# Performance work log

Hardware: AMD Instinct MI355X
Metric: run time of the kernel (lower is better)

Reference implementation:

```python
import jax, jax.numpy as jnp
import numpy as np

B, C, H, W = 4, 64, 128, 128
D_INNER, D_STATE, DT_RANK, K = 192, 16, 6, 4  # d_model = 3*C//2 = 96, expand = 2
EPS = 1e-5


def _haar():
    # pywt db1: dec_lo=[s,s], dec_hi=[-s,s]; code reverses dec_* and uses rec_* in
    # original order -> for Haar both dec and rec filter banks are identical.
    s = np.float32(1.0 / np.sqrt(2.0))
    lo = np.array([s, s], np.float32)
    hi = np.array([s, -s], np.float32)
    # stack order: [lo(i)lo(j), hi(i)lo(j), lo(i)hi(j), hi(i)hi(j)]
    return np.stack([np.outer(lo, lo), np.outer(hi, lo),
                     np.outer(lo, hi), np.outer(hi, hi)], 0)  # (4,2,2)

DEC = jnp.asarray(_haar())
REC = jnp.asarray(_haar())
DN = ('NCHW', 'OIHW', 'NCHW')


def _ln(x, s, b):
    m = x.mean(-1, keepdims=True)
    v = x.var(-1, keepdims=True)
    return (x - m) * jax.lax.rsqrt(v + EPS) * s + b


def _wt(x):
    b, c, h, w = x.shape
    wf = jnp.tile(DEC[:, None], (c, 1, 1, 1))  # (4c,1,2,2), groups=c, pad=0 for db1
    y = jax.lax.conv_general_dilated(x, wf, (2, 2), 'VALID',
                                     feature_group_count=c, dimension_numbers=DN)
    return y.reshape(b, c, 4, h // 2, w // 2)


def _iwt(x):
    # conv_transpose2d(stride=2, pad=0, groups=c) == lhs-dilated conv with flipped kernel, pad k-1
    b, c = x.shape[0], x.shape[1]
    h2, w2 = x.shape[3], x.shape[4]
    xr = x.reshape(b, c * 4, h2, w2)
    wf = jnp.tile(REC[:, ::-1, ::-1][None], (c, 1, 1, 1))  # (c,4,2,2)
    return jax.lax.conv_general_dilated(xr, wf, (1, 1), ((1, 1), (1, 1)),
                                        lhs_dilation=(2, 2), feature_group_count=c,
                                        dimension_numbers=DN)


def _ss2d(x, in_proj_w, conv_dw_w, conv_dw_b, x_proj_w, dt_proj_w, dt_proj_b,
          A_log, Ds, out_norm_s, out_norm_b, out_proj_w):
    b, d, h, w = x.shape  # d == D_INNER
    L = h * w
    xz = jnp.einsum('bchw,ec->behw', x, in_proj_w)  # (b,2d,h,w)
    x1, z = xz[:, :d], xz[:, d:]
    x1 = jax.lax.conv_general_dilated(x1, conv_dw_w, (1, 1), ((1, 1), (1, 1)),
                                      feature_group_count=d, dimension_numbers=DN)
    x1 = jax.nn.silu(x1 + conv_dw_b[None, :, None, None])
    # 4-direction flattening: hw, wh, and their reverses
    xf = x1.reshape(b, d, L)
    xt = x1.transpose(0, 1, 3, 2).reshape(b, d, L)
    xs = jnp.stack([xf, xt], 1)
    xs = jnp.concatenate([xs, xs[..., ::-1]], 1)  # (b,K,d,L)
    x_dbl = jnp.einsum('bkdl,kcd->bkcl', xs, x_proj_w)
    dts = x_dbl[:, :, :DT_RANK]
    Bs = x_dbl[:, :, DT_RANK:DT_RANK + D_STATE]   # (b,K,n,L)
    Cs = x_dbl[:, :, DT_RANK + D_STATE:]
    delta = jax.nn.softplus(jnp.einsum('bkrl,kdr->bkdl', dts, dt_proj_w)
                            + dt_proj_b[None, :, :, None])
    A = -jnp.exp(A_log)  # (K,d,n)

    def step(hc, inp):
        d_t, u_t, b_t, c_t = inp  # (b,K,d),(b,K,d),(b,K,n),(b,K,n)
        dA = jnp.exp(d_t[..., None] * A[None])
        hc = hc * dA + (d_t * u_t)[..., None] * b_t[:, :, None, :]
        y = jnp.einsum('bkdn,bkn->bkd', hc, c_t)
        return hc, y

    h0 = jnp.zeros((b, K, d, D_STATE), x.dtype)
    inputs = (delta.transpose(3, 0, 1, 2), xs.transpose(3, 0, 1, 2),
              Bs.transpose(3, 0, 1, 2), Cs.transpose(3, 0, 1, 2))
    _, ys = jax.lax.scan(step, h0, inputs)            # (L,b,K,d)
    out_y = ys.transpose(1, 2, 3, 0) + xs * Ds[None, :, :, None]  # (b,K,d,L)
    inv_y = out_y[:, 2:][..., ::-1]
    wh = out_y[:, 1].reshape(b, d, w, h).transpose(0, 1, 3, 2).reshape(b, d, L)
    invwh = inv_y[:, 1].reshape(b, d, w, h).transpose(0, 1, 3, 2).reshape(b, d, L)
    y = out_y[:, 0] + inv_y[:, 0] + wh + invwh        # (b,d,L)
    y = _ln(y.reshape(b, d, h, w).transpose(0, 2, 3, 1), out_norm_s, out_norm_b)
    y = y * jax.nn.silu(z.transpose(0, 2, 3, 1))
    y = jnp.einsum('bhwd,ed->bhwe', y, out_proj_w)
    return y.transpose(0, 3, 1, 2)


def reference(x, wt_low_scale, wt_high_scale, low_conv_w, in_proj_w, conv_dw_w,
              conv_dw_b, x_proj_w, dt_proj_w, dt_proj_b, A_log, Ds,
              out_norm_s, out_norm_b, out_proj_w, ln2_s, ln2_b, eca_w):
    b, c = x.shape[0], x.shape[1]
    wt = _wt(x)                                       # (b,c,4,h2,w2)
    h2, w2 = wt.shape[3], wt.shape[4]
    low = wt[:, :, 0] * wt_low_scale
    high = wt[:, :, 1:].reshape(b, c * 3, h2, w2) * wt_high_scale
    low = jax.nn.silu(jnp.einsum('bchw,ec->behw', low, low_conv_w[:, :, 0, 0]))
    high = _ss2d(high, in_proj_w, conv_dw_w, conv_dw_b, x_proj_w, dt_proj_w,
                 dt_proj_b, A_log, Ds, out_norm_s, out_norm_b, out_proj_w)
    high = _ln(high.transpose(0, 2, 3, 1), ln2_s, ln2_b).transpose(0, 3, 1, 2)
    mamba = jnp.tile(low, (1, 3, 1, 1)) * high
    merged = jnp.concatenate([low, mamba], 1).reshape(b, c, 4, h2, w2)
    y = _iwt(merged)                                  # (b,c,h,w)
    # ECA: gap -> conv1d(k=5) over channels -> sigmoid gate
    pooled = y.mean((2, 3))[:, None, :]               # (b,1,c)
    att = jax.lax.conv_general_dilated(pooled, eca_w.reshape(1, 1, 5), (1,),
                                       ((2, 2),), dimension_numbers=('NCH', 'OIH', 'NCH'))
    att = jax.nn.sigmoid(att[:, 0])
    return y * att[:, :, None, None] + x


def setup_inputs():
    key = jax.random.key(0)
    ks = jax.random.split(key, 20)
    f = jax.random.normal
    return {
        'x': f(ks[0], (B, C, H, W), jnp.float32),
        'wt_low_scale': jax.random.uniform(ks[1], (1, C, 1, 1), jnp.float32),
        'wt_high_scale': jax.random.uniform(ks[2], (1, 3 * C, 1, 1), jnp.float32),
        'low_conv_w': f(ks[3], (C, C, 1, 1), jnp.float32) * 0.1,
        'in_proj_w': f(ks[4], (2 * D_INNER, D_INNER), jnp.float32) * 0.05,
        'conv_dw_w': f(ks[5], (D_INNER, 1, 3, 3), jnp.float32) * 0.3,
        'conv_dw_b': f(ks[6], (D_INNER,), jnp.float32) * 0.1,
        'x_proj_w': f(ks[7], (K, DT_RANK + 2 * D_STATE, D_INNER), jnp.float32) * 0.05,
        'dt_proj_w': f(ks[8], (K, D_INNER, DT_RANK), jnp.float32) * 0.1,
        'dt_proj_b': jax.random.uniform(ks[9], (K, D_INNER), jnp.float32) - 4.0,
        'A_log': jax.random.uniform(ks[10], (K, D_INNER, D_STATE), jnp.float32),
        'Ds': f(ks[11], (K, D_INNER), jnp.float32) * 0.1,
        'out_norm_s': jnp.ones((D_INNER,), jnp.float32),
        'out_norm_b': jnp.zeros((D_INNER,), jnp.float32),
        'out_proj_w': f(ks[12], (D_INNER, D_INNER), jnp.float32) * 0.05,
        'ln2_s': jnp.ones((3 * C,), jnp.float32),
        'ln2_b': jnp.zeros((3 * C,), jnp.float32),
        'eca_w': f(ks[13], (5,), jnp.float32) * 0.3,
    }
```

## Files before the change

kernel.cpp:

```cpp
#include <hip/hip_runtime.h>

constexpr int cB = 4, cC = 64, cH = 128, cW = 128;
constexpr int cL = 4096;
constexpr int cD = 192, cN = 16;
constexpr int NCH = 64, CHUNK = 64;

__device__ __forceinline__ float silu_f(float v) { return v / (1.f + __expf(-v)); }

__global__ __launch_bounds__(256) void k_wt(const float* __restrict__ x,
                                            const float* __restrict__ wls,
                                            const float* __restrict__ whs,
                                            float* __restrict__ lraw,
                                            float* __restrict__ high) {
    int idx = blockIdx.x * 256 + threadIdx.x;
    int j = idx & 63, i = (idx >> 6) & 63, c = (idx >> 12) & 63, b = idx >> 18;
    const float* xp = x + (((size_t)(b * cC + c)) * cH + 2 * i) * cW + 2 * j;
    float x00 = xp[0], x01 = xp[1], x10 = xp[cW], x11 = xp[cW + 1];
    float s0 = 0.5f * (x00 + x01 + x10 + x11);
    float s1 = 0.5f * (x00 + x01 - x10 - x11);
    float s2 = 0.5f * (x00 - x01 + x10 - x11);
    float s3 = 0.5f * (x00 - x01 - x10 + x11);
    int l = i * 64 + j;
    lraw[(size_t)(b * cC + c) * cL + l] = s0 * wls[c];
    int ch = c * 3;
    high[(size_t)(b * cD + ch + 0) * cL + l] = s1 * whs[ch + 0];
    high[(size_t)(b * cD + ch + 1) * cL + l] = s2 * whs[ch + 1];
    high[(size_t)(b * cD + ch + 2) * cL + l] = s3 * whs[ch + 2];
}

__global__ __launch_bounds__(256) void k_lowconv(const float* __restrict__ lraw,
                                                 const float* __restrict__ w,
                                                 float* __restrict__ lowT) {
    int bid = blockIdx.x;
    int lt0 = (bid & 63) * 64;
    int b = bid >> 6;
    __shared__ float sW[16][68];
    __shared__ float sI[16][65];
    int tid = threadIdx.x, lt = tid & 63, eg = tid >> 6;
    float acc[16];
#pragma unroll
    for (int m = 0; m < 16; m++) acc[m] = 0.f;
    for (int c0 = 0; c0 < 64; c0 += 16) {
#pragma unroll
        for (int q = 0; q < 4; q++) {
            int tt = tid + q * 256;
            int cc = tt & 15, ee = tt >> 4;
            sW[cc][ee] = w[ee * 64 + c0 + cc];
        }
#pragma unroll
        for (int q = 0; q < 4; q++) {
            int tt = tid + q * 256;
            int ll = tt & 63, cc = tt >> 6;
            sI[cc][ll] = lraw[(size_t)(b * cC + c0 + cc) * cL + lt0 + ll];
        }
        __syncthreads();
#pragma unroll
        for (int cc = 0; cc < 16; cc++) {
            float iv = sI[cc][lt];
#pragma unroll
            for (int m = 0; m < 16; m++) acc[m] = fmaf(sW[cc][eg * 16 + m], iv, acc[m]);
        }
        __syncthreads();
    }
#pragma unroll
    for (int m = 0; m < 16; m++) {
        int e = eg * 16 + m;
        lowT[((size_t)b * cL + lt0 + lt) * 64 + e] = silu_f(acc[m]);
    }
}

__global__ __launch_bounds__(256) void k_inproj(const float* __restrict__ hi,
                                                const float* __restrict__ w,
                                                float* __restrict__ xout,
                                                float* __restrict__ zT) {
    int bid = blockIdx.x;
    int et = bid % 6;
    int blt = bid / 6;
    int lt0 = (blt & 63) * 64;
    int b = blt >> 6;
    int e0 = et * 64;
    __shared__ float sW[16][68];
    __shared__ float sI[16][65];
    int tid = threadIdx.x, lt = tid & 63, eg = tid >> 6;
    float acc[16];
#pragma unroll
    for (int m = 0; m < 16; m++) acc[m] = 0.f;
    for (int c0 = 0; c0 < 192; c0 += 16) {
#pragma unroll
        for (int q = 0; q < 4; q++) {
            int tt = tid + q * 256;
            int cc = tt & 15, ee = tt >> 4;
            sW[cc][ee] = w[(e0 + ee) * 192 + c0 + cc];
        }
#pragma unroll
        for (int q = 0; q < 4; q++) {
            int tt = tid + q * 256;
            int ll = tt & 63, cc = tt >> 6;
            sI[cc][ll] = hi[(size_t)(b * cD + c0 + cc) * cL + lt0 + ll];
        }
        __syncthreads();
#pragma unroll
        for (int cc = 0; cc < 16; cc++) {
            float iv = sI[cc][lt];
#pragma unroll
            for (int m = 0; m < 16; m++) acc[m] = fmaf(sW[cc][eg * 16 + m], iv, acc[m]);
        }
        __syncthreads();
    }
#pragma unroll
    for (int m = 0; m < 16; m++) {
        int e = e0 + eg * 16 + m;
        float v = acc[m];
        if (e < 192) xout[(size_t)(b * cD + e) * cL + lt0 + lt] = v;
        else zT[((size_t)b * cL + lt0 + lt) * 192 + (e - 192)] = v;
    }
}

__global__ __launch_bounds__(256) void k_dwconv(const float* __restrict__ xin,
                                                const float* __restrict__ w,
                                                const float* __restrict__ bias,
                                                float* __restrict__ x1,
                                                float* __restrict__ u1) {
    int bd = blockIdx.x;
    int d = bd % cD;
    const float* xp = xin + (size_t)bd * cL;
    float wv[9];
#pragma unroll
    for (int t = 0; t < 9; t++) wv[t] = w[d * 9 + t];
    float bv = bias[d];
    __shared__ float sm[64][65];
    int tid = threadIdx.x;
#pragma unroll
    for (int q = 0; q < 16; q++) {
        int p = tid + q * 256;
        int i = p >> 6, j = p & 63;
        float acc = bv;
#pragma unroll
        for (int di = 0; di < 3; di++) {
            int ii = i + di - 1;
            if (ii < 0 || ii >= 64) continue;
#pragma unroll
            for (int dj = 0; dj < 3; dj++) {
                int jj = j + dj - 1;
                if (jj < 0 || jj >= 64) continue;
                acc = fmaf(wv[di * 3 + dj], xp[ii * 64 + jj], acc);
            }
        }
        sm[i][j] = silu_f(acc);
    }
    __syncthreads();
#pragma unroll
    for (int q = 0; q < 16; q++) {
        int p = tid + q * 256;
        x1[(size_t)bd * cL + p] = sm[p >> 6][p & 63];
        u1[(size_t)bd * cL + p] = sm[p & 63][p >> 6];
    }
}

__global__ __launch_bounds__(256) void k_xproj(const float* __restrict__ x1,
                                               const float* __restrict__ u1,
                                               const float* __restrict__ xpw,
                                               float* __restrict__ xdbl) {
    int bid = blockIdx.x;
    int lt0 = (bid & 63) * 64;
    int k = (bid >> 6) & 3;
    int b = bid >> 8;
    const float* src = (k & 1) ? u1 : x1;
    bool rev = (k >= 2);
    __shared__ float sW[16][68];
    __shared__ float sI[16][65];
    int tid = threadIdx.x, lt = tid & 63, eg = tid >> 6;
    float acc[16];
#pragma unroll
    for (int m = 0; m < 16; m++) acc[m] = 0.f;
    for (int c0 = 0; c0 < 192; c0 += 16) {
#pragma unroll
        for (int q = 0; q < 4; q++) {
            int tt = tid + q * 256;
            int cc = tt & 15, ee = tt >> 4;
            sW[cc][ee] = (ee < 38) ? xpw[(k * 38 + ee) * 192 + c0 + cc] : 0.f;
        }
#pragma unroll
        for (int q = 0; q < 4; q++) {
            int tt = tid + q * 256;
            int ll = tt & 63, cc = tt >> 6;
            int l = lt0 + ll;
            int lm = rev ? (cL - 1 - l) : l;
            sI[cc][ll] = src[(size_t)(b * cD + c0 + cc) * cL + lm];
        }
        __syncthreads();
#pragma unroll
        for (int cc = 0; cc < 16; cc++) {
            float iv = sI[cc][lt];
#pragma unroll
            for (int m = 0; m < 16; m++) acc[m] = fmaf(sW[cc][eg * 16 + m], iv, acc[m]);
        }
        __syncthreads();
    }
#pragma unroll
    for (int m = 0; m < 16; m++) {
        int e = eg * 16 + m;
        if (e < 38) xdbl[(size_t)((b * 4 + k) * 38 + e) * cL + lt0 + lt] = acc[m];
    }
}

__global__ __launch_bounds__(192) void k_scan1(const float* __restrict__ xdbl,
                                               const float* __restrict__ x1,
                                               const float* __restrict__ u1,
                                               const float* __restrict__ dtw,
                                               const float* __restrict__ dtb,
                                               const float* __restrict__ alog,
                                               float* __restrict__ P,
                                               float* __restrict__ S) {
    int bid = blockIdx.x;
    int ch = bid % NCH;
    int bk = bid / NCH;
    int k = bk & 3, b = bk >> 2;
    int tid = threadIdx.x;
    int d = tid;
    float Av2[16], h[16];
#pragma unroll
    for (int j = 0; j < 16; j++) {
        Av2[j] = -__expf(alog[(k * 192 + d) * 16 + j]) * 1.44269504088896f;
        h[j] = 0.f;
    }
    float dtbv = dtb[k * 192 + d];
    float dtwv[6];
#pragma unroll
    for (int r = 0; r < 6; r++) dtwv[r] = dtw[(k * 192 + d) * 6 + r];
    const float* dtrows = xdbl + (size_t)(bk * 38) * cL;
    const float* Brow = xdbl + (size_t)(bk * 38 + 6) * cL;
    const float* ubase = ((k & 1) ? u1 : x1) + ((size_t)b * cD + d) * cL;
    bool rev = (k >= 2);

    __shared__ float sB[2][16][16];
    __shared__ float sdt[2][16][8];

    int rowA = tid >> 4, colA = tid & 15;
    int p0 = ch * CHUNK;

    for (int idx = tid; idx < 256; idx += 192)
        sB[0][idx & 15][idx >> 4] = Brow[(size_t)(idx >> 4) * cL + p0 + (idx & 15)];
    if (tid < 96) sdt[0][colA][rowA] = dtrows[(size_t)rowA * cL + p0 + colA];

    float Q = 0.f;
    int cur = 0;
    for (int t0 = p0; t0 < p0 + CHUNK; t0 += 16) {
        __syncthreads();
        if (t0 + 16 < p0 + CHUNK) {
            int t1 = t0 + 16;
            for (int idx = tid; idx < 256; idx += 192)
                sB[cur ^ 1][idx & 15][idx >> 4] = Brow[(size_t)(idx >> 4) * cL + t1 + (idx & 15)];
            if (tid < 96) sdt[cur ^ 1][colA][rowA] = dtrows[(size_t)rowA * cL + t1 + colA];
        }
        float uvals[16];
        {
            const float* up = rev ? (ubase + (cL - 16 - t0)) : (ubase + t0);
#pragma unroll
            for (int q = 0; q < 4; q++)
                *reinterpret_cast<float4*>(&uvals[q * 4]) = *reinterpret_cast<const float4*>(up + q * 4);
        }
#pragma unroll
        for (int l = 0; l < 16; l++) {
            float acc = dtbv;
#pragma unroll
            for (int r = 0; r < 6; r++) acc = fmaf(dtwv[r], sdt[cur][l][r], acc);
            float sp = fmaxf(acc, 0.f) + __logf(1.f + __expf(-fabsf(acc)));
            Q += sp;
            float uv = rev ? uvals[15 - l] : uvals[l];
            float duB = sp * uv;
            float Bv[16];
            *reinterpret_cast<float4*>(&Bv[0])  = *reinterpret_cast<const float4*>(&sB[cur][l][0]);
            *reinterpret_cast<float4*>(&Bv[4])  = *reinterpret_cast<const float4*>(&sB[cur][l][4]);
            *reinterpret_cast<float4*>(&Bv[8])  = *reinterpret_cast<const float4*>(&sB[cur][l][8]);
            *reinterpret_cast<float4*>(&Bv[12]) = *reinterpret_cast<const float4*>(&sB[cur][l][12]);
#pragma unroll
            for (int j = 0; j < 16; j++)
                h[j] = fmaf(h[j], exp2f(sp * Av2[j]), duB * Bv[j]);
        }
        cur ^= 1;
    }
    size_t base = (size_t)bid * 16 * 192 + d;
#pragma unroll
    for (int j = 0; j < 16; j++) {
        P[base + (size_t)j * 192] = exp2f(Av2[j] * Q);
        S[base + (size_t)j * 192] = h[j];
    }
}

__global__ __launch_bounds__(256) void k_carry(const float* __restrict__ P,
                                               float* __restrict__ S) {
    int gid = blockIdx.x * 256 + threadIdx.x;
    int d = gid % 192;
    int n = (gid / 192) & 15;
    int bk = gid / 3072;
    float h = 0.f;
    for (int c = 0; c < NCH; c++) {
        size_t idx = ((size_t)(bk * NCH + c) * 16 + n) * 192 + d;
        h = fmaf(P[idx], h, S[idx]);
        S[idx] = h;
    }
}

__global__ __launch_bounds__(192) void k_scan2(const float* __restrict__ xdbl,
                                               const float* __restrict__ x1,
                                               const float* __restrict__ u1,
                                               const float* __restrict__ dtw,
                                               const float* __restrict__ dtb,
                                               const float* __restrict__ alog,
                                               const float* __restrict__ dss,
                                               const float* __restrict__ S,
                                               float* __restrict__ yacc) {
    int bid = blockIdx.x;
    int ch = bid % NCH;
    int bk = bid / NCH;
    int k = bk & 3, b = bk >> 2;
    int tid = threadIdx.x;
    int d = tid;
    float Av2[16], h[16];
#pragma unroll
    for (int j = 0; j < 16; j++) {
        Av2[j] = -__expf(alog[(k * 192 + d) * 16 + j]) * 1.44269504088896f;
        h[j] = (ch == 0) ? 0.f : S[((size_t)(bk * NCH + ch - 1) * 16 + j) * 192 + d];
    }
    float Dv = dss[k * 192 + d];
    float dtbv = dtb[k * 192 + d];
    float dtwv[6];
#pragma unroll
    for (int r = 0; r < 6; r++) dtwv[r] = dtw[(k * 192 + d) * 6 + r];
    const float* dtrows = xdbl + (size_t)(bk * 38) * cL;
    const float* Brow = xdbl + (size_t)(bk * 38 + 6) * cL;
    const float* Crow = xdbl + (size_t)(bk * 38 + 22) * cL;
    const float* ubase = ((k & 1) ? u1 : x1) + ((size_t)b * cD + d) * cL;
    bool rev = (k >= 2);

    __shared__ float sB[2][16][16];
    __shared__ float sC[2][16][16];
    __shared__ float sdt[2][16][8];

    int rowA = tid >> 4, colA = tid & 15;
    int p0 = ch * CHUNK;

    for (int idx = tid; idx < 256; idx += 192) {
        sB[0][idx & 15][idx >> 4] = Brow[(size_t)(idx >> 4) * cL + p0 + (idx & 15)];
        sC[0][idx & 15][idx >> 4] = Crow[(size_t)(idx >> 4) * cL + p0 + (idx & 15)];
    }
    if (tid < 96) sdt[0][colA][rowA] = dtrows[(size_t)rowA * cL + p0 + colA];

    int cur = 0;
    for (int t0 = p0; t0 < p0 + CHUNK; t0 += 16) {
        __syncthreads();
        if (t0 + 16 < p0 + CHUNK) {
            int t1 = t0 + 16;
            for (int idx = tid; idx < 256; idx += 192) {
                sB[cur ^ 1][idx & 15][idx >> 4] = Brow[(size_t)(idx >> 4) * cL + t1 + (idx & 15)];
                sC[cur ^ 1][idx & 15][idx >> 4] = Crow[(size_t)(idx >> 4) * cL + t1 + (idx & 15)];
            }
            if (tid < 96) sdt[cur ^ 1][colA][rowA] = dtrows[(size_t)rowA * cL + t1 + colA];
        }
        float uvals[16];
        {
            const float* up = rev ? (ubase + (cL - 16 - t0)) : (ubase + t0);
#pragma unroll
            for (int q = 0; q < 4; q++)
                *reinterpret_cast<float4*>(&uvals[q * 4]) = *reinterpret_cast<const float4*>(up + q * 4);
        }
#pragma unroll
        for (int l = 0; l < 16; l++) {
            float acc = dtbv;
#pragma unroll
            for (int r = 0; r < 6; r++) acc = fmaf(dtwv[r], sdt[cur][l][r], acc);
            float sp = fmaxf(acc, 0.f) + __logf(1.f + __expf(-fabsf(acc)));
            float uv = rev ? uvals[15 - l] : uvals[l];
            float duB = sp * uv;
            float Bv[16], Cv[16];
            *reinterpret_cast<float4*>(&Bv[0])  = *reinterpret_cast<const float4*>(&sB[cur][l][0]);
            *reinterpret_cast<float4*>(&Bv[4])  = *reinterpret_cast<const float4*>(&sB[cur][l][4]);
            *reinterpret_cast<float4*>(&Bv[8])  = *reinterpret_cast<const float4*>(&sB[cur][l][8]);
            *reinterpret_cast<float4*>(&Bv[12]) = *reinterpret_cast<const float4*>(&sB[cur][l][12]);
            *reinterpret_cast<float4*>(&Cv[0])  = *reinterpret_cast<const float4*>(&sC[cur][l][0]);
            *reinterpret_cast<float4*>(&Cv[4])  = *reinterpret_cast<const float4*>(&sC[cur][l][4]);
            *reinterpret_cast<float4*>(&Cv[8])  = *reinterpret_cast<const float4*>(&sC[cur][l][8]);
            *reinterpret_cast<float4*>(&Cv[12]) = *reinterpret_cast<const float4*>(&sC[cur][l][12]);
            float yA = 0.f, yB = 0.f;
#pragma unroll
            for (int j = 0; j < 8; j++) {
                h[j] = fmaf(h[j], exp2f(sp * Av2[j]), duB * Bv[j]);
                yA = fmaf(h[j], Cv[j], yA);
            }
#pragma unroll
            for (int j = 8; j < 16; j++) {
                h[j] = fmaf(h[j], exp2f(sp * Av2[j]), duB * Bv[j]);
                yB = fmaf(h[j], Cv[j], yB);
            }
            float y = yA + yB + uv * Dv;
            int lg = t0 + l;
            int lm;
            if (k == 0) lm = lg;
            else if (k == 1) lm = (lg & 63) * 64 + (lg >> 6);
            else if (k == 2) lm = cL - 1 - lg;
            else { int qq = cL - 1 - lg; lm = (qq & 63) * 64 + (qq >> 6); }
            atomicAdd(&yacc[((size_t)b * cL + lm) * 192 + d], y);
        }
        cur ^= 1;
    }
}

__global__ __launch_bounds__(256) void k_comb(const float* __restrict__ yacc,
                                              const float* __restrict__ zT,
                                              const float* __restrict__ ons,
                                              const float* __restrict__ onb,
                                              float* __restrict__ yln) {
    int bid = blockIdx.x;
    int b = bid >> 10;
    int pg = bid & 1023;
    int tid = threadIdx.x;
    int wq = tid >> 6, lane = tid & 63;
    int l = pg * 4 + wq;
    float v[3];
    float s = 0.f, s2 = 0.f;
#pragma unroll
    for (int m = 0; m < 3; m++) {
        int d = lane + 64 * m;
        float t = yacc[((size_t)b * cL + l) * 192 + d];
        v[m] = t;
        s += t;
        s2 += t * t;
    }
#pragma unroll
    for (int o = 1; o < 64; o <<= 1) {
        s += __shfl_xor(s, o);
        s2 += __shfl_xor(s2, o);
    }
    float mean = s / 192.f;
    float var = s2 / 192.f - mean * mean;
    float rstd = rsqrtf(var + 1e-5f);
#pragma unroll
    for (int m = 0; m < 3; m++) {
        int d = lane + 64 * m;
        float zv = zT[((size_t)b * cL + l) * 192 + d];
        float yn = (v[m] - mean) * rstd * ons[d] + onb[d];
        yln[((size_t)b * cL + l) * 192 + d] = yn * silu_f(zv);
    }
}

__global__ __launch_bounds__(256) void k_outproj(const float* __restrict__ yln,
                                                 const float* __restrict__ w,
                                                 float* __restrict__ hout) {
    int bid = blockIdx.x;
    int lt0 = (bid & 63) * 64;
    int et = (bid >> 6) % 3;
    int b = bid / 192;
    int e0 = et * 64;
    __shared__ float sW[16][68];
    __shared__ float sI[16][65];
    int tid = threadIdx.x, lt = tid & 63, eg = tid >> 6;
    float acc[16];
#pragma unroll
    for (int m = 0; m < 16; m++) acc[m] = 0.f;
    for (int c0 = 0; c0 < 192; c0 += 16) {
#pragma unroll
        for (int q = 0; q < 4; q++) {
            int tt = tid + q * 256;
            int cc = tt & 15, ee = tt >> 4;
            sW[cc][ee] = w[(e0 + ee) * 192 + c0 + cc];
        }
#pragma unroll
        for (int q = 0; q < 4; q++) {
            int tt = tid + q * 256;
            int cc = tt & 15, lq = tt >> 4;
            sI[cc][lq] = yln[((size_t)b * cL + lt0 + lq) * 192 + c0 + cc];
        }
        __syncthreads();
#pragma unroll
        for (int cc = 0; cc < 16; cc++) {
            float iv = sI[cc][lt];
#pragma unroll
            for (int m = 0; m < 16; m++) acc[m] = fmaf(sW[cc][eg * 16 + m], iv, acc[m]);
        }
        __syncthreads();
    }
#pragma unroll
    for (int m = 0; m < 16; m++) {
        hout[((size_t)b * cL + lt0 + lt) * 192 + e0 + eg * 16 + m] = acc[m];
    }
}

__global__ __launch_bounds__(256) void k_ln2(const float* __restrict__ hout,
                                             const float* __restrict__ lowT,
                                             const float* __restrict__ l2s,
                                             const float* __restrict__ l2b,
                                             float* __restrict__ merged) {
    int bid = blockIdx.x;
    int b = bid >> 10;
    int pg = bid & 1023;
    int tid = threadIdx.x;
    int wq = tid >> 6, lane = tid & 63;
    int l = pg * 4 + wq;
    float v[3];
    float s = 0.f, s2 = 0.f;
#pragma unroll
    for (int m = 0; m < 3; m++) {
        int d = lane + 64 * m;
        float t = hout[((size_t)b * cL + l) * 192 + d];
        v[m] = t;
        s += t;
        s2 += t * t;
    }
#pragma unroll
    for (int o = 1; o < 64; o <<= 1) {
        s += __shfl_xor(s, o);
        s2 += __shfl_xor(s2, o);
    }
    float mean = s / 192.f;
    float var = s2 / 192.f - mean * mean;
    float rstd = rsqrtf(var + 1e-5f);
    float lv = lowT[((size_t)b * cL + l) * 64 + lane];
    float* mp = merged + ((size_t)b * cL + l) * 256;
    mp[lane] = lv;
#pragma unroll
    for (int m = 0; m < 3; m++) {
        int d = lane + 64 * m;
        float hn = (v[m] - mean) * rstd * l2s[d] + l2b[d];
        mp[64 + d] = lv * hn;
    }
}

__global__ __launch_bounds__(256) void k_iwt(const float* __restrict__ merged,
                                             float* __restrict__ ypre) {
    int idx = blockIdx.x * 256 + threadIdx.x;
    int j = idx & 63, i = (idx >> 6) & 63, g = (idx >> 12) & 63, b = idx >> 18;
    const float4 mv = *reinterpret_cast<const float4*>(merged + ((size_t)b * cL + i * 64 + j) * 256 + g * 4);
    float m0 = mv.x, m1 = mv.y, m2 = mv.z, m3 = mv.w;
    float* yp = ypre + ((size_t)(b * 64 + g) * cH + 2 * i) * cW + 2 * j;
    float2 r0 = make_float2(0.5f * (m0 + m1 + m2 + m3), 0.5f * (m0 + m1 - m2 - m3));
    float2 r1 = make_float2(0.5f * (m0 - m1 + m2 - m3), 0.5f * (m0 - m1 - m2 + m3));
    *reinterpret_cast<float2*>(yp) = r0;
    *reinterpret_cast<float2*>(yp + cW) = r1;
}

__global__ __launch_bounds__(256) void k_pool(const float* __restrict__ ypre,
                                              float* __restrict__ pooled) {
    int bg = blockIdx.x;
    const float* p = ypre + (size_t)bg * (cH * cW);
    float s = 0.f;
    for (int t = threadIdx.x; t < cH * cW; t += 256) s += p[t];
#pragma unroll
    for (int o = 1; o < 64; o <<= 1) s += __shfl_xor(s, o);
    __shared__ float red[4];
    if ((threadIdx.x & 63) == 0) red[threadIdx.x >> 6] = s;
    __syncthreads();
    if (threadIdx.x == 0) pooled[bg] = (red[0] + red[1] + red[2] + red[3]) * (1.f / (cH * cW));
}

__global__ __launch_bounds__(256) void k_eca(const float* __restrict__ pooled,
                                             const float* __restrict__ w,
                                             float* __restrict__ att) {
    int t = threadIdx.x;
    int b = t >> 6, c = t & 63;
    float s = 0.f;
#pragma unroll
    for (int u = 0; u < 5; u++) {
        int cc = c + u - 2;
        if (cc >= 0 && cc < 64) s += w[u] * pooled[b * 64 + cc];
    }
    att[t] = 1.f / (1.f + __expf(-s));
}

__global__ __launch_bounds__(256) void k_final(const float* __restrict__ ypre,
                                               const float* __restrict__ x,
                                               const float* __restrict__ att,
                                               float* __restrict__ out) {
    int idx = blockIdx.x * 256 + threadIdx.x;
    size_t base = (size_t)idx * 4;
    int bc = (int)(base >> 14);
    float a = att[bc];
    float4 yv = *reinterpret_cast<const float4*>(ypre + base);
    float4 xv = *reinterpret_cast<const float4*>(x + base);
    float4 o;
    o.x = fmaf(yv.x, a, xv.x);
    o.y = fmaf(yv.y, a, xv.y);
    o.z = fmaf(yv.z, a, xv.z);
    o.w = fmaf(yv.w, a, xv.w);
    *reinterpret_cast<float4*>(out + base) = o;
}

extern "C" void kernel_launch(void* const* d_in, const int* in_sizes, int n_in,
                              void* d_out, int out_size, void* d_ws, size_t ws_size,
                              hipStream_t stream) {
    const float* x    = (const float*)d_in[0];
    const float* wls  = (const float*)d_in[1];
    const float* whs  = (const float*)d_in[2];
    const float* lcw  = (const float*)d_in[3];
    const float* ipw  = (const float*)d_in[4];
    const float* dww  = (const float*)d_in[5];
    const float* dwb  = (const float*)d_in[6];
    const float* xpw  = (const float*)d_in[7];
    const float* dtw  = (const float*)d_in[8];
    const float* dtb  = (const float*)d_in[9];
    const float* alog = (const float*)d_in[10];
    const float* dss  = (const float*)d_in[11];
    const float* ons  = (const float*)d_in[12];
    const float* onb  = (const float*)d_in[13];
    const float* opw  = (const float*)d_in[14];
    const float* l2s  = (const float*)d_in[15];
    const float* l2b  = (const float*)d_in[16];
    const float* ecw  = (const float*)d_in[17];
    float* out = (float*)d_out;
    float* w = (float*)d_ws;

    float* high   = w + 0;
    float* lraw   = w + 3145728;
    float* lowT   = w + 4194304;
    float* xbuf   = w + 5242880;
    float* zT     = w + 8388608;
    float* x1     = w + 11534336;
    float* u1     = w + 14680064;
    float* yacc   = w + 17825792;
    float* Sbuf   = w + 20971520;
    float* xdbl   = high;
    float* Pbuf   = xbuf;
    float* yln    = xbuf;
    float* hout   = high;
    float* merged = x1;
    float* ypre   = yacc;
    float* pooled = lraw;
    float* att    = lraw + 256;

    k_wt<<<4096, 256, 0, stream>>>(x, wls, whs, lraw, high);
    k_lowconv<<<256, 256, 0, stream>>>(lraw, lcw, lowT);
    k_inproj<<<1536, 256, 0, stream>>>(high, ipw, xbuf, zT);
    k_dwconv<<<768, 256, 0, stream>>>(xbuf, dww, dwb, x1, u1);
    k_xproj<<<1024, 256, 0, stream>>>(x1, u1, xpw, xdbl);
    hipMemsetAsync(yacc, 0, (size_t)cB * cL * cD * sizeof(float), stream);
    k_scan1<<<1024, 192, 0, stream>>>(xdbl, x1, u1, dtw, dtb, alog, Pbuf, Sbuf);
    k_carry<<<192, 256, 0, stream>>>(Pbuf, Sbuf);
    k_scan2<<<1024, 192, 0, stream>>>(xdbl, x1, u1, dtw, dtb, alog, dss, Sbuf, yacc);
    k_comb<<<4096, 256, 0, stream>>>(yacc, zT, ons, onb, yln);
    k_outproj<<<768, 256, 0, stream>>>(yln, opw, hout);
    k_ln2<<<4096, 256, 0, stream>>>(hout, lowT, l2s, l2b, merged);
    k_iwt<<<4096, 256, 0, stream>>>(merged, ypre);
    k_pool<<<256, 256, 0, stream>>>(ypre, pooled);
    k_eca<<<1, 256, 0, stream>>>(pooled, ecw, att);
    k_final<<<4096, 256, 0, stream>>>(ypre, x, att, out);
}
```

Before: 414.3 us.

## Halve scan chunk size, preload whole chunk, recompute decay in carry pass

The chunked selective scan now uses 128 chunks of 32 steps instead of 64 chunks of 64, doubling the block count for the two scan kernels. Each block loads its whole B/C/dt tile and u values up front with one barrier, replacing the double-buffered inner loop. The first scan writes only the per-channel sum Q instead of 16 decay products, and the carry kernel recomputes exp2(A*Q). This trades a longer serial carry loop and a doubled S buffer for more parallelism and less P traffic.

Result: slower. 493.5 us (+19.1%).

```diff
diff --git a/kernel.cpp b/kernel.cpp
--- a/kernel.cpp
+++ b/kernel.cpp
@@ -3,7 +3,7 @@
 constexpr int cB = 4, cC = 64, cH = 128, cW = 128;
 constexpr int cL = 4096;
 constexpr int cD = 192, cN = 16;
-constexpr int NCH = 64, CHUNK = 64;
+constexpr int NCH = 128, CHUNK = 32;
 
 __device__ __forceinline__ float silu_f(float v) { return v / (1.f + __expf(-v)); }
 
@@ -210,7 +210,7 @@
                                                const float* __restrict__ dtw,
                                                const float* __restrict__ dtb,
                                                const float* __restrict__ alog,
-                                               float* __restrict__ P,
+                                               float* __restrict__ Qb,
                                                float* __restrict__ S) {
     int bid = blockIdx.x;
     int ch = bid % NCH;
@@ -218,6 +218,28 @@
     int k = bk & 3, b = bk >> 2;
     int tid = threadIdx.x;
     int d = tid;
+    bool rev = (k >= 2);
+    const float* dtrows = xdbl + (size_t)(bk * 38) * cL;
+    const float* Brow = xdbl + (size_t)(bk * 38 + 6) * cL;
+    const float* ubase = ((k & 1) ? u1 : x1) + ((size_t)b * cD + d) * cL;
+    int p0 = ch * CHUNK;
+
+    __shared__ float sB[32][16];
+    __shared__ float sdt[32][8];
+
+    for (int idx = tid; idx < 512; idx += 192)
+        sB[idx & 31][idx >> 5] = Brow[(size_t)(idx >> 5) * cL + p0 + (idx & 31)];
+    if (tid < 192) {
+        int r = tid >> 5, cc = tid & 31;
+        if (r < 6) sdt[cc][r] = dtrows[(size_t)r * cL + p0 + cc];
+    }
+    float u[32];
+    {
+        const float* up = rev ? (ubase + (cL - 32 - p0)) : (ubase + p0);
+#pragma unroll
+        for (int q = 0; q < 8; q++)
+            *reinterpret_cast<float4*>(&u[q * 4]) = *reinterpret_cast<const float4*>(up + q * 4);
+    }
     float Av2[16], h[16];
 #pragma unroll
     for (int j = 0; j < 16; j++) {
@@ -228,76 +250,47 @@
     float dtwv[6];
 #pragma unroll
     for (int r = 0; r < 6; r++) dtwv[r] = dtw[(k * 192 + d) * 6 + r];
-    const float* dtrows = xdbl + (size_t)(bk * 38) * cL;
-    const float* Brow = xdbl + (size_t)(bk * 38 + 6) * cL;
-    const float* ubase = ((k & 1) ? u1 : x1) + ((size_t)b * cD + d) * cL;
-    bool rev = (k >= 2);
-
-    __shared__ float sB[2][16][16];
-    __shared__ float sdt[2][16][8];
-
-    int rowA = tid >> 4, colA = tid & 15;
-    int p0 = ch * CHUNK;
-
-    for (int idx = tid; idx < 256; idx += 192)
-        sB[0][idx & 15][idx >> 4] = Brow[(size_t)(idx >> 4) * cL + p0 + (idx & 15)];
-    if (tid < 96) sdt[0][colA][rowA] = dtrows[(size_t)rowA * cL + p0 + colA];
+    __syncthreads();
 
     float Q = 0.f;
-    int cur = 0;
-    for (int t0 = p0; t0 < p0 + CHUNK; t0 += 16) {
-        __syncthreads();
-        if (t0 + 16 < p0 + CHUNK) {
-            int t1 = t0 + 16;
-            for (int idx = tid; idx < 256; idx += 192)
-                sB[cur ^ 1][idx & 15][idx >> 4] = Brow[(size_t)(idx >> 4) * cL + t1 + (idx & 15)];
-            if (tid < 96) sdt[cur ^ 1][colA][rowA] = dtrows[(size_t)rowA * cL + t1 + colA];
-        }
-        float uvals[16];
-        {
-            const float* up = rev ? (ubase + (cL - 16 - t0)) : (ubase + t0);
-#pragma unroll
-            for (int q = 0; q < 4; q++)
-                *reinterpret_cast<float4*>(&uvals[q * 4]) = *reinterpret_cast<const float4*>(up + q * 4);
-        }
-#pragma unroll
-        for (int l = 0; l < 16; l++) {
-            float acc = dtbv;
-#pragma unroll
-            for (int r = 0; r < 6; r++) acc = fmaf(dtwv[r], sdt[cur][l][r], acc);
-            float sp = fmaxf(acc, 0.f) + __logf(1.f + __expf(-fabsf(acc)));
-            Q += sp;
-            float uv = rev ? uvals[15 - l] : uvals[l];
-            float duB = sp * uv;
-            float Bv[16];
-            *reinterpret_cast<float4*>(&Bv[0])  = *reinterpret_cast<const float4*>(&sB[cur][l][0]);
-            *reinterpret_cast<float4*>(&Bv[4])  = *reinterpret_cast<const float4*>(&sB[cur][l][4]);
-            *reinterpret_cast<float4*>(&Bv[8])  = *reinterpret_cast<const float4*>(&sB[cur][l][8]);
-            *reinterpret_cast<float4*>(&Bv[12]) = *reinterpret_cast<const float4*>(&sB[cur][l][12]);
-#pragma unroll
-            for (int j = 0; j < 16; j++)
-                h[j] = fmaf(h[j], exp2f(sp * Av2[j]), duB * Bv[j]);
-        }
-        cur ^= 1;
+#pragma unroll
+    for (int l = 0; l < 32; l++) {
+        float acc = dtbv;
+#pragma unroll
+        for (int r = 0; r < 6; r++) acc = fmaf(dtwv[r], sdt[l][r], acc);
+        float sp = fmaxf(acc, 0.f) + __logf(1.f + __expf(-fabsf(acc)));
+        Q += sp;
+        float uv = rev ? u[31 - l] : u[l];
+        float duB = sp * uv;
+        float Bv[16];
+        *reinterpret_cast<float4*>(&Bv[0])  = *reinterpret_cast<const float4*>(&sB[l][0]);
+        *reinterpret_cast<float4*>(&Bv[4])  = *reinterpret_cast<const float4*>(&sB[l][4]);
+        *reinterpret_cast<float4*>(&Bv[8])  = *reinterpret_cast<const float4*>(&sB[l][8]);
+        *reinterpret_cast<float4*>(&Bv[12]) = *reinterpret_cast<const float4*>(&sB[l][12]);
+#pragma unroll
+        for (int j = 0; j < 16; j++)
+            h[j] = fmaf(h[j], exp2f(sp * Av2[j]), duB * Bv[j]);
     }
     size_t base = (size_t)bid * 16 * 192 + d;
 #pragma unroll
-    for (int j = 0; j < 16; j++) {
-        P[base + (size_t)j * 192] = exp2f(Av2[j] * Q);
-        S[base + (size_t)j * 192] = h[j];
-    }
-}
-
-__global__ __launch_bounds__(256) void k_carry(const float* __restrict__ P,
-                                               float* __restrict__ S) {
+    for (int j = 0; j < 16; j++) S[base + (size_t)j * 192] = h[j];
+    Qb[(size_t)bid * 192 + d] = Q;
+}
+
+__global__ __launch_bounds__(256) void k_carryQ(const float* __restrict__ alog,
+                                                const float* __restrict__ Qb,
+                                                float* __restrict__ S) {
     int gid = blockIdx.x * 256 + threadIdx.x;
     int d = gid % 192;
     int n = (gid / 192) & 15;
     int bk = gid / 3072;
+    int k = bk & 3;
+    float Av2 = -__expf(alog[(k * 192 + d) * 16 + n]) * 1.44269504088896f;
     float h = 0.f;
     for (int c = 0; c < NCH; c++) {
+        size_t qidx = (size_t)(bk * NCH + c) * 192 + d;
         size_t idx = ((size_t)(bk * NCH + c) * 16 + n) * 192 + d;
-        h = fmaf(P[idx], h, S[idx]);
+        h = fmaf(exp2f(Av2 * Qb[qidx]), h, S[idx]);
         S[idx] = h;
     }
 }
@@ -317,92 +310,81 @@
     int k = bk & 3, b = bk >> 2;
     int tid = threadIdx.x;
     int d = tid;
-    float Av2[16], h[16];
-#pragma unroll
-    for (int j = 0; j < 16; j++) {
-        Av2[j] = -__expf(alog[(k * 192 + d) * 16 + j]) * 1.44269504088896f;
-        h[j] = (ch == 0) ? 0.f : S[((size_t)(bk * NCH + ch - 1) * 16 + j) * 192 + d];
-    }
-    float Dv = dss[k * 192 + d];
-    float dtbv = dtb[k * 192 + d];
-    float dtwv[6];
-#pragma unroll
-    for (int r = 0; r < 6; r++) dtwv[r] = dtw[(k * 192 + d) * 6 + r];
+    bool rev = (k >= 2);
     const float* dtrows = xdbl + (size_t)(bk * 38) * cL;
     const float* Brow = xdbl + (size_t)(bk * 38 + 6) * cL;
     const float* Crow = xdbl + (size_t)(bk * 38 + 22) * cL;
     const float* ubase = ((k & 1) ? u1 : x1) + ((size_t)b * cD + d) * cL;
-    bool rev = (k >= 2);
-
-    __shared__ float sB[2][16][16];
-    __shared__ float sC[2][16][16];
-    __shared__ float sdt[2][16][8];
-
-    int rowA = tid >> 4, colA = tid & 15;
     int p0 = ch * CHUNK;
 
-    for (int idx = tid; idx < 256; idx += 192) {
-        sB[0][idx & 15][idx >> 4] = Brow[(size_t)(idx >> 4) * cL + p0 + (idx & 15)];
-        sC[0][idx & 15][idx >> 4] = Crow[(size_t)(idx >> 4) * cL + p0 + (idx & 15)];
-    }
-    if (tid < 96) sdt[0][colA][rowA] = dtrows[(size_t)rowA * cL + p0 + colA];
-
-    int cur = 0;
-    for (int t0 = p0; t0 < p0 + CHUNK; t0 += 16) {
-        __syncthreads();
-        if (t0 + 16 < p0 + CHUNK) {
-            int t1 = t0 + 16;
-            for (int idx = tid; idx < 256; idx += 192) {
-                sB[cur ^ 1][idx & 15][idx >> 4] = Brow[(size_t)(idx >> 4) * cL + t1 + (idx & 15)];
-                sC[cur ^ 1][idx & 15][idx >> 4] = Crow[(size_t)(idx >> 4) * cL + t1 + (idx & 15)];
-            }
-            if (tid < 96) sdt[cur ^ 1][colA][rowA] = dtrows[(size_t)rowA * cL + t1 + colA];
-        }
-        float uvals[16];
-        {
-            const float* up = rev ? (ubase + (cL - 16 - t0)) : (ubase + t0);
-#pragma unroll
-            for (int q = 0; q < 4; q++)
-                *reinterpret_cast<float4*>(&uvals[q * 4]) = *reinterpret_cast<const float4*>(up + q * 4);
-        }
-#pragma unroll
-        for (int l = 0; l < 16; l++) {
-            float acc = dtbv;
-#pragma unroll
-            for (int r = 0; r < 6; r++) acc = fmaf(dtwv[r], sdt[cur][l][r], acc);
-            float sp = fmaxf(acc, 0.f) + __logf(1.f + __expf(-fabsf(acc)));
-            float uv = rev ? uvals[15 - l] : uvals[l];
-            float duB = sp * uv;
-            float Bv[16], Cv[16];
-            *reinterpret_cast<float4*>(&Bv[0])  = *reinterpret_cast<const float4*>(&sB[cur][l][0]);
-            *reinterpret_cast<float4*>(&Bv[4])  = *reinterpret_cast<const float4*>(&sB[cur][l][4]);
-            *reinterpret_cast<float4*>(&Bv[8])  = *reinterpret_cast<const float4*>(&sB[cur][l][8]);
-            *reinterpret_cast<float4*>(&Bv[12]) = *reinterpret_cast<const float4*>(&sB[cur][l][12]);
-            *reinterpret_cast<float4*>(&Cv[0])  = *reinterpret_cast<const float4*>(&sC[cur][l][0]);
-            *reinterpret_cast<float4*>(&Cv[4])  = *reinterpret_cast<const float4*>(&sC[cur][l][4]);
-            *reinterpret_cast<float4*>(&Cv[8])  = *reinterpret_cast<const float4*>(&sC[cur][l][8]);
-            *reinterpret_cast<float4*>(&Cv[12]) = *reinterpret_cast<const float4*>(&sC[cur][l][12]);
-            float yA = 0.f, yB = 0.f;
-#pragma unroll
-            for (int j = 0; j < 8; j++) {
-                h[j] = fmaf(h[j], exp2f(sp * Av2[j]), duB * Bv[j]);
-                yA = fmaf(h[j], Cv[j], yA);
-            }
-#pragma unroll
-            for (int j = 8; j < 16; j++) {
-                h[j] = fmaf(h[j], exp2f(sp * Av2[j]), duB * Bv[j]);
-                yB = fmaf(h[j], Cv[j], yB);
-            }
-            float y = yA + yB + uv * Dv;
-            int lg = t0 + l;
-            int lm;
-            if (k == 0) lm = lg;
-            else if (k == 1) lm = (lg & 63) * 64 + (lg >> 6);
-            else if (k == 2) lm = cL - 1 - lg;
-            else { int qq = cL - 1 - lg; lm = (qq & 63) * 64 + (qq >> 6); }
-            atomicAdd(&yacc[((size_t)b * cL + lm) * 192 + d], y);
-        }
-        cur ^= 1;
+    __shared__ float sB[32][16];
+    __shared__ float sC[32][16];
+    __shared__ float sdt[32][8];
+
+    for (int idx = tid; idx < 512; idx += 192) {
+        sB[idx & 31][idx >> 5] = Brow[(size_t)(idx >> 5) * cL + p0 + (idx & 31)];
+        sC[idx & 31][idx >> 5] = Crow[(size_t)(idx >> 5) * cL + p0 + (idx & 31)];
+    }
+    if (tid < 192) {
+        int r = tid >> 5, cc = tid & 31;
+        if (r < 6) sdt[cc][r] = dtrows[(size_t)r * cL + p0 + cc];
+    }
+    float u[32];
+    {
+        const float* up = rev ? (ubase + (cL - 32 - p0)) : (ubase + p0);
+#pragma unroll
+        for (int q = 0; q < 8; q++)
+            *reinterpret_cast<float4*>(&u[q * 4]) = *reinterpret_cast<const float4*>(up + q * 4);
+    }
+    float Av2[16], h[16];
+#pragma unroll
+    for (int j = 0; j < 16; j++) {
+        Av2[j] = -__expf(alog[(k * 192 + d) * 16 + j]) * 1.44269504088896f;
+        h[j] = (ch == 0) ? 0.f : S[((size_t)(bk * NCH + ch - 1) * 16 + j) * 192 + d];
+    }
+    float Dv = dss[k * 192 + d];
+    float dtbv = dtb[k * 192 + d];
+    float dtwv[6];
+#pragma unroll
+    for (int r = 0; r < 6; r++) dtwv[r] = dtw[(k * 192 + d) * 6 + r];
+    __syncthreads();
+
+#pragma unroll
+    for (int l = 0; l < 32; l++) {
+        float acc = dtbv;
+#pragma unroll
+        for (int r = 0; r < 6; r++) acc = fmaf(dtwv[r], sdt[l][r], acc);
+        float sp = fmaxf(acc, 0.f) + __logf(1.f + __expf(-fabsf(acc)));
+        float uv = rev ? u[31 - l] : u[l];
+        float duB = sp * uv;
+        float Bv[16], Cv[16];
+        *reinterpret_cast<float4*>(&Bv[0])  = *reinterpret_cast<const float4*>(&sB[l][0]);
+        *reinterpret_cast<float4*>(&Bv[4])  = *reinterpret_cast<const float4*>(&sB[l][4]);
+        *reinterpret_cast<float4*>(&Bv[8])  = *reinterpret_cast<const float4*>(&sB[l][8]);
+        *reinterpret_cast<float4*>(&Bv[12]) = *reinterpret_cast<const float4*>(&sB[l][12]);
+        *reinterpret_cast<float4*>(&Cv[0])  = *reinterpret_cast<const float4*>(&sC[l][0]);
+        *reinterpret_cast<float4*>(&Cv[4])  = *reinterpret_cast<const float4*>(&sC[l][4]);
+        *reinterpret_cast<float4*>(&Cv[8])  = *reinterpret_cast<const float4*>(&sC[l][8]);
+        *reinterpret_cast<float4*>(&Cv[12]) = *reinterpret_cast<const float4*>(&sC[l][12]);
+        float yA = 0.f, yB = 0.f;
+#pragma unroll
+        for (int j = 0; j < 8; j++) {
+            h[j] = fmaf(h[j], exp2f(sp * Av2[j]), duB * Bv[j]);
+            yA = fmaf(h[j], Cv[j], yA);
+        }
+#pragma unroll
+        for (int j = 8; j < 16; j++) {
+            h[j] = fmaf(h[j], exp2f(sp * Av2[j]), duB * Bv[j]);
+            yB = fmaf(h[j], Cv[j], yB);
+        }
+        float y = yA + yB + uv * Dv;
+        int lg = p0 + l;
+        int lm;
+        if (k == 0) lm = lg;
+        else if (k == 1) lm = (lg & 63) * 64 + (lg >> 6);
+        else if (k == 2) lm = cL - 1 - lg;
+        else { int qq = cL - 1 - lg; lm = (qq & 63) * 64 + (qq >> 6); }
+        atomicAdd(&yacc[((size_t)b * cL + lm) * 192 + d], y);
     }
 }
 
@@ -618,8 +600,8 @@
     float* u1     = w + 14680064;
     float* yacc   = w + 17825792;
     float* Sbuf   = w + 20971520;
+    float* Qbuf   = w + 27262976;
     float* xdbl   = high;
-    float* Pbuf   = xbuf;
     float* yln    = xbuf;
     float* hout   = high;
     float* merged = x1;
@@ -633,9 +615,9 @@
     k_dwconv<<<768, 256, 0, stream>>>(xbuf, dww, dwb, x1, u1);
     k_xproj<<<1024, 256, 0, stream>>>(x1, u1, xpw, xdbl);
     hipMemsetAsync(yacc, 0, (size_t)cB * cL * cD * sizeof(float), stream);
-    k_scan1<<<1024, 192, 0, stream>>>(xdbl, x1, u1, dtw, dtb, alog, Pbuf, Sbuf);
-    k_carry<<<192, 256, 0, stream>>>(Pbuf, Sbuf);
-    k_scan2<<<1024, 192, 0, stream>>>(xdbl, x1, u1, dtw, dtb, alog, dss, Sbuf, yacc);
+    k_scan1<<<2048, 192, 0, stream>>>(xdbl, x1, u1, dtw, dtb, alog, Qbuf, Sbuf);
+    k_carryQ<<<192, 256, 0, stream>>>(alog, Qbuf, Sbuf);
+    k_scan2<<<2048, 192, 0, stream>>>(xdbl, x1, u1, dtw, dtb, alog, dss, Sbuf, yacc);
     k_comb<<<4096, 256, 0, stream>>>(yacc, zT, ons, onb, yln);
     k_outproj<<<768, 256, 0, stream>>>(yln, opw, hout);
     k_ln2<<<4096, 256, 0, stream>>>(hout, lowT, l2s, l2b, merged);
```
